# Kernel tuning notes

Hardware: AMD Instinct MI355X
Metric: run time of the kernel (lower is better)

Reference implementation:

```python
import jax, jax.numpy as jnp
import numpy as np

D_MODEL = 1024
NUM_HEADS = 16
D_K = D_MODEL // NUM_HEADS
THETA = 10000.0
BATCH = 2
SEQ = 2048


def setup_inputs() -> dict:
    key = jax.random.key(0)
    ks = jax.random.split(key, 5)
    std = np.sqrt(2.0 / (D_MODEL + D_MODEL))
    return {
        "x": jax.random.normal(ks[0], (BATCH, SEQ, D_MODEL), dtype=jnp.float32),
        "Wq": jax.random.normal(ks[1], (D_MODEL, D_MODEL), dtype=jnp.float32) * std,
        "Wk": jax.random.normal(ks[2], (D_MODEL, D_MODEL), dtype=jnp.float32) * std,
        "Wv": jax.random.normal(ks[3], (D_MODEL, D_MODEL), dtype=jnp.float32) * std,
        "Wo": jax.random.normal(ks[4], (D_MODEL, D_MODEL), dtype=jnp.float32) * std,
        "token_positions": jnp.arange(SEQ, dtype=jnp.int64),
    }


def _apply_rope(t, cos, sin):
    # t: [B, H, S, D_K]; cos/sin: [S, D_K//2]
    # Block-diag 2x2 rotation on consecutive pairs (2k, 2k+1) == elementwise rotation.
    tr = t.reshape(*t.shape[:-1], D_K // 2, 2)
    t0, t1 = tr[..., 0], tr[..., 1]
    o0 = t0 * cos - t1 * sin
    o1 = t0 * sin + t1 * cos
    return jnp.stack([o0, o1], axis=-1).reshape(t.shape)


def reference(x, Wq, Wk, Wv, Wo, token_positions):
    B, S, _ = x.shape
    # projections: custom Linear does x @ W.T
    def split_heads(t):
        return t.reshape(B, S, NUM_HEADS, D_K).transpose(0, 2, 1, 3)  # [B,H,S,Dk]

    q = split_heads(x @ Wq.T)
    k = split_heads(x @ Wk.T)
    v = split_heads(x @ Wv.T)

    # RoPE angle table: theta_ik = pos / THETA**(2k/d_k)
    inv_freq = 1.0 / (THETA ** (2.0 * jnp.arange(D_K // 2, dtype=jnp.float32) / D_K))
    angles = token_positions.astype(jnp.float32)[:, None] * inv_freq[None, :]  # [S, Dk//2]
    cos, sin = jnp.cos(angles), jnp.sin(angles)

    q = _apply_rope(q, cos, sin)
    k = _apply_rope(k, cos, sin)

    scale = 1.0 / np.sqrt(D_K)
    scores = jnp.einsum("bhqd,bhkd->bhqk", q, k) * scale  # [B,H,S,S]
    causal = jnp.tril(jnp.ones((S, S), dtype=bool))
    scores = jnp.where(causal, scores, -jnp.inf)
    attn = jax.nn.softmax(scores, axis=-1)
    out = jnp.einsum("bhqk,bhkd->bhqd", attn, v)  # [B,H,S,Dk]
    out = out.transpose(0, 2, 1, 3).reshape(B, S, D_MODEL)
    return out @ Wo.T
```

## Files before the change

### kernel.cpp

```cpp
#include <hip/hip_runtime.h>
#include <hip/hip_bf16.h>
#include <cstdint>
#include <cstddef>

#define BATCH 2
#define SEQ   2048
#define DM    1024
#define NH    16
#define DK    64
#define LOG2E 1.4426950408889634f

typedef __attribute__((ext_vector_type(8)))  short short8;
typedef __attribute__((ext_vector_type(4)))  float f32x4;
typedef __attribute__((ext_vector_type(16))) float f32x16;
typedef __attribute__((ext_vector_type(4)))  int   i32x4;
typedef __attribute__((ext_vector_type(2)))  int   i32x2;

__device__ __forceinline__ void gload_lds16(const __hip_bfloat16* g, __hip_bfloat16* l) {
  __builtin_amdgcn_global_load_lds((const __attribute__((address_space(1))) void*)g,
                                   (__attribute__((address_space(3))) void*)l, 16, 0, 0);
}

__device__ __forceinline__ int cvtpk_bf16(float lo, float hi) {
  int r;
  asm("v_cvt_pk_bf16_f32 %0, %1, %2" : "=v"(r) : "v"(lo), "v"(hi));
  return r;
}

__device__ __forceinline__ float bf2f(short v) {
  return __int_as_float(((int)(unsigned short)v) << 16);
}

__device__ __forceinline__ float partner32(float x, int hi) {
  auto r = __builtin_amdgcn_permlane32_swap(__float_as_int(x), __float_as_int(x), false, false);
  return __int_as_float(hi ? r[0] : r[1]);
}

__global__ void cast_all(const float* __restrict__ x,  const float* __restrict__ Wq,
                         const float* __restrict__ Wk, const float* __restrict__ Wv,
                         const float* __restrict__ Wo, __hip_bfloat16* __restrict__ dst,
                         const int* __restrict__ pos,  float2* __restrict__ tbl) {
  const int NX = BATCH * SEQ * DM;
  int t = blockIdx.x * 256 + threadIdx.x;
  if (t < SEQ * 32) {
    int s = t >> 5, d2 = t & 31;
    float ang = (float)pos[s] * exp2f(-(float)d2 * 0.415241011860920f);
    float cv, sv;
    __sincosf(ang, &sv, &cv);
    tbl[t] = make_float2(cv, sv);
  }
  size_t i = (size_t)t * 4;
  const float* s;
  if (i < (size_t)NX) {
    s = x + i;
  } else {
    size_t j = i - NX;
    int wsel = (int)(j >> 20);
    size_t o = j & ((1u << 20) - 1);
    s = (wsel == 0 ? Wq : wsel == 1 ? Wk : wsel == 2 ? Wv : Wo) + o;
  }
  float4 v = *(const float4*)s;
  i32x2 pk;
  pk[0] = cvtpk_bf16(v.x, v.y);
  pk[1] = cvtpk_bf16(v.z, v.w);
  *(i32x2*)(dst + i) = pk;
}

template<bool F32OUT, bool VSPLIT>
__global__ __launch_bounds__(256)
void gemm_bt(const __hip_bfloat16* __restrict__ A,
             const __hip_bfloat16* __restrict__ Bw,
             void* __restrict__ Cv, __hip_bfloat16* __restrict__ vt,
             int M, int N, int K, int ldc) {
  __shared__ __hip_bfloat16 As[2][128 * 32];
  __shared__ __hip_bfloat16 Bs[2][128 * 32];
  const int tid  = threadIdx.x;
  const int lane = tid & 63;
  const int w    = tid >> 6;
  const int wr   = w >> 1, wc = w & 1;
  const int g    = lane >> 4;
  const int lr   = lane & 15;

  const int nwg = gridDim.x * gridDim.y;
  const int bid = blockIdx.y * gridDim.x + blockIdx.x;
  const int cpx = nwg >> 3;
  const int sbid = (bid & 7) * cpx + (bid >> 3);
  const int bx = sbid % gridDim.x, by = sbid / gridDim.x;
  const int bm0  = by * 128;
  const int bn0  = bx * 128;

  f32x4 acc[4][4] = {};

  const int strow = lane >> 2;
  const int stcol = (lane & 3) * 8;

  auto STAGE = [&](int buf, int kt) {
    #pragma unroll
    for (int it = 0; it < 2; ++it) {
      int row = (w * 2 + it) * 16 + strow;
      gload_lds16(A  + (size_t)(bm0 + row) * K + kt + stcol, &As[buf][row * 32 + stcol]);
      gload_lds16(Bw + (size_t)(bn0 + row) * K + kt + stcol, &Bs[buf][row * 32 + stcol]);
    }
  };

  STAGE(0, 0);
  __syncthreads();
  int cur = 0;
  const int nk = K / 32;
  for (int ki = 0; ki < nk; ++ki) {
    if (ki + 1 < nk) STAGE(cur ^ 1, (ki + 1) * 32);
    short8 a[4], b[4];
    #pragma unroll
    for (int m = 0; m < 4; ++m)
      a[m] = *(const short8*)(&As[cur][(wr * 64 + m * 16 + lr) * 32 + g * 8]);
    #pragma unroll
    for (int n = 0; n < 4; ++n)
      b[n] = *(const short8*)(&Bs[cur][(wc * 64 + n * 16 + lr) * 32 + g * 8]);
    #pragma unroll
    for (int m = 0; m < 4; ++m)
      #pragma unroll
      for (int n = 0; n < 4; ++n)
        acc[m][n] = __builtin_amdgcn_mfma_f32_16x16x32_bf16(a[m], b[n], acc[m][n], 0, 0, 0);
    __syncthreads();
    cur ^= 1;
  }

  if (VSPLIT && bn0 >= 2048) {
    #pragma unroll
    for (int m = 0; m < 4; ++m)
      #pragma unroll
      for (int n = 0; n < 4; ++n) {
        int nn = bn0 + wc * 64 + n * 16 + lr - 2048;
        int hd = nn >> 6, d = nn & 63;
        int m0 = bm0 + wr * 64 + m * 16 + g * 4;
        int bb = m0 >> 11, ss = m0 & 2047;
        i32x2 pk;
        pk[0] = cvtpk_bf16(acc[m][n][0], acc[m][n][1]);
        pk[1] = cvtpk_bf16(acc[m][n][2], acc[m][n][3]);
        *(i32x2*)(vt + ((size_t)(bb * NH + hd) * DK + d) * SEQ + ss) = pk;
      }
  } else {
    #pragma unroll
    for (int m = 0; m < 4; ++m)
      #pragma unroll
      for (int n = 0; n < 4; ++n) {
        int col = bn0 + wc * 64 + n * 16 + lr;
        #pragma unroll
        for (int r = 0; r < 4; ++r) {
          int row = bm0 + wr * 64 + m * 16 + g * 4 + r;
          float v = acc[m][n][r];
          if (F32OUT) ((float*)Cv)[(size_t)row * ldc + col] = v;
          else        ((__hip_bfloat16*)Cv)[(size_t)row * ldc + col] = __float2bfloat16(v);
        }
      }
  }
}

__global__ void rope_vec(__hip_bfloat16* __restrict__ qk, const float2* __restrict__ tbl) {
  int idx = blockIdx.x * 256 + threadIdx.x;
  int row = idx >> 7;
  int hg  = idx & 127;
  int h   = hg >> 3, gg = hg & 7;
  const float QS = 0.125f * LOG2E;
  size_t base = (size_t)row * 2048 + h * 64 + gg * 8;
  const float2* tp = tbl + (row & (SEQ - 1)) * 32 + gg * 4;
  short8 q = *(const short8*)(qk + base);
  short8 k = *(const short8*)(qk + base + 1024);
  i32x4 qo, ko;
  #pragma unroll
  for (int j = 0; j < 4; ++j) {
    float2 cs = tp[j];
    float q0 = bf2f(q[2 * j]), q1 = bf2f(q[2 * j + 1]);
    float k0 = bf2f(k[2 * j]), k1 = bf2f(k[2 * j + 1]);
    qo[j] = cvtpk_bf16((q0 * cs.x - q1 * cs.y) * QS, (q0 * cs.y + q1 * cs.x) * QS);
    ko[j] = cvtpk_bf16(k0 * cs.x - k1 * cs.y,        k0 * cs.y + k1 * cs.x);
  }
  *(i32x4*)(qk + base)        = qo;
  *(i32x4*)(qk + base + 1024) = ko;
}

__global__ __launch_bounds__(512)
void flash_attn(const __hip_bfloat16* __restrict__ qk,
                const __hip_bfloat16* __restrict__ vt,
                __hip_bfloat16* __restrict__ outb) {
  __shared__ __hip_bfloat16 Kls[2][2][64 * 64];
  __shared__ __hip_bfloat16 Vls[2][2][64 * 64];
  const int pi = blockIdx.x;
  const int NQB = SEQ / 128;
  const int qbh = NQB - 1 - pi, qbl = pi;
  const int hd = blockIdx.y, b = blockIdx.z;
  const int tid = threadIdx.x, lane = tid & 63, w = tid >> 6;
  const int wh = w & 3;
  const int qb_eff = (w < 4) ? qbh : qbl;
  const int hi = lane >> 5, ql = lane & 31;
  const int q0w = qb_eff * 128 + wh * 32;
  const int nph  = qbh + 1;
  const int tmaxw = 2 * qb_eff + (wh >> 1);

  const __hip_bfloat16* Qb = qk + (size_t)(b * SEQ) * 2048 + hd * DK;
  const __hip_bfloat16* Kg = qk + (size_t)(b * SEQ) * 2048 + 1024 + hd * DK;
  const __hip_bfloat16* Vg = vt + (size_t)(b * NH + hd) * DK * SEQ;

  short8 qf[4];
  #pragma unroll
  for (int c = 0; c < 4; ++c)
    qf[c] = *(const short8*)(Qb + (size_t)(q0w + ql) * 2048 + c * 16 + hi * 8);

  f32x16 o0 = {}, o1 = {};
  float m_run = -1e30f, l_run = 0.f;

  const int srow = tid >> 3;
  const int sc0  = (tid & 7) * 8;
  const int swz  = (srow & 7) << 3;

  short8 kr0, kr1, vr0, vr1;
  auto LOAD = [&](int ph) {
    int r0 = ph * 128;
    kr0 = *(const short8*)(Kg + (size_t)(r0 + srow) * 2048 + sc0);
    kr1 = *(const short8*)(Kg + (size_t)(r0 + 64 + srow) * 2048 + sc0);
    vr0 = *(const short8*)(Vg + (size_t)srow * SEQ + r0 + sc0);
    vr1 = *(const short8*)(Vg + (size_t)srow * SEQ + r0 + 64 + sc0);
  };
  auto WRITE = [&](int buf) {
    *(short8*)(&Kls[buf][0][srow * 64 + (sc0 ^ swz)]) = kr0;
    *(short8*)(&Kls[buf][1][srow * 64 + (sc0 ^ swz)]) = kr1;
    *(short8*)(&Vls[buf][0][srow * 64 + (sc0 ^ swz)]) = vr0;
    *(short8*)(&Vls[buf][1][srow * 64 + (sc0 ^ swz)]) = vr1;
  };

  LOAD(0);
  WRITE(0);

  for (int ph = 0; ph < nph; ++ph) {
    const int cur = ph & 1;
    if (ph + 1 < nph) LOAD(ph + 1);
    __syncthreads();

    #pragma unroll
    for (int sub = 0; sub < 2; ++sub) {
      const int tt = 2 * ph + sub;
      if (tt <= tmaxw) {
        f32x16 s0 = {}, s1 = {};
        __builtin_amdgcn_s_setprio(1);
        #pragma unroll
        for (int c = 0; c < 4; ++c) {
          int col = (c * 16 + hi * 8) ^ ((ql & 7) << 3);
          short8 ka = *(const short8*)(&Kls[cur][sub][ql * 64 + col]);
          short8 kb = *(const short8*)(&Kls[cur][sub][(32 + ql) * 64 + col]);
          s0 = __builtin_amdgcn_mfma_f32_32x32x16_bf16(ka, qf[c], s0, 0, 0, 0);
          s1 = __builtin_amdgcn_mfma_f32_32x32x16_bf16(kb, qf[c], s1, 0, 0, 0);
        }
        __builtin_amdgcn_s_setprio(0);

        if (tt * 64 + 63 > q0w) {
          int qg = q0w + ql;
          #pragma unroll
          for (int r = 0; r < 16; ++r) {
            int krow = (r & 3) + 8 * (r >> 2) + 4 * hi;
            if (tt * 64 + krow > qg)      s0[r] = -1e30f;
            if (tt * 64 + 32 + krow > qg) s1[r] = -1e30f;
          }
        }

        float mx = s0[0];
        #pragma unroll
        for (int r = 1; r < 16; ++r) mx = fmaxf(mx, s0[r]);
        #pragma unroll
        for (int r = 0; r < 16; ++r) mx = fmaxf(mx, s1[r]);
        mx = fmaxf(mx, partner32(mx, hi));

        if (!__all(mx <= m_run + 8.f)) {
          float mn  = fmaxf(m_run, mx);
          float fac = __builtin_amdgcn_exp2f(m_run - mn);
          m_run = mn;
          l_run *= fac;
          #pragma unroll
          for (int r = 0; r < 16; ++r) { o0[r] *= fac; o1[r] *= fac; }
        }
        float sum = 0.f;
        #pragma unroll
        for (int r = 0; r < 16; ++r) { s0[r] = __builtin_amdgcn_exp2f(s0[r] - m_run); sum += s0[r]; }
        #pragma unroll
        for (int r = 0; r < 16; ++r) { s1[r] = __builtin_amdgcn_exp2f(s1[r] - m_run); sum += s1[r]; }
        sum += partner32(sum, hi);
        l_run += sum;

        short8 pf[4];
        #pragma unroll
        for (int kt = 0; kt < 2; ++kt) {
          const f32x16& sv = kt ? s1 : s0;
          #pragma unroll
          for (int u = 0; u < 2; ++u) {
            int wa0 = cvtpk_bf16(sv[8 * u + 0], sv[8 * u + 1]);
            int wa1 = cvtpk_bf16(sv[8 * u + 2], sv[8 * u + 3]);
            int wb0 = cvtpk_bf16(sv[8 * u + 4], sv[8 * u + 5]);
            int wb1 = cvtpk_bf16(sv[8 * u + 6], sv[8 * u + 7]);
            auto r0 = __builtin_amdgcn_permlane32_swap(wa0, wb0, false, false);
            auto r1 = __builtin_amdgcn_permlane32_swap(wa1, wb1, false, false);
            i32x4 fr; fr[0] = r0[0]; fr[1] = r1[0]; fr[2] = r0[1]; fr[3] = r1[1];
            pf[kt * 2 + u] = *(short8*)&fr;
          }
        }

        __builtin_amdgcn_s_setprio(1);
        #pragma unroll
        for (int cc = 0; cc < 4; ++cc) {
          int col = (cc * 16 + hi * 8) ^ ((ql & 7) << 3);
          short8 va = *(const short8*)(&Vls[cur][sub][ql * 64 + col]);
          short8 vb = *(const short8*)(&Vls[cur][sub][(32 + ql) * 64 + col]);
          o0 = __builtin_amdgcn_mfma_f32_32x32x16_bf16(va, pf[cc], o0, 0, 0, 0);
          o1 = __builtin_amdgcn_mfma_f32_32x32x16_bf16(vb, pf[cc], o1, 0, 0, 0);
        }
        __builtin_amdgcn_s_setprio(0);
      }
    }

    if (ph + 1 < nph) WRITE(cur ^ 1);
  }

  float inv = 1.f / l_run;
  __hip_bfloat16* orow = outb + (size_t)(b * SEQ + q0w + ql) * DM + hd * DK;
  #pragma unroll
  for (int dt = 0; dt < 2; ++dt) {
    const f32x16& oa = dt ? o1 : o0;
    #pragma unroll
    for (int a = 0; a < 4; ++a) {
      int d0 = dt * 32 + a * 8 + hi * 4;
      i32x2 pk;
      pk[0] = cvtpk_bf16(oa[4 * a + 0] * inv, oa[4 * a + 1] * inv);
      pk[1] = cvtpk_bf16(oa[4 * a + 2] * inv, oa[4 * a + 3] * inv);
      *(i32x2*)(orow + d0) = pk;
    }
  }
}

extern "C" void kernel_launch(void* const* d_in, const int* in_sizes, int n_in,
                              void* d_out, int out_size, void* d_ws, size_t ws_size,
                              hipStream_t stream) {
  const float* x  = (const float*)d_in[0];
  const float* Wq = (const float*)d_in[1];
  const float* Wk = (const float*)d_in[2];
  const float* Wv = (const float*)d_in[3];
  const float* Wo = (const float*)d_in[4];
  const int*   tp = (const int*)d_in[5];
  float* out = (float*)d_out;

  char* ws = (char*)d_ws;
  __hip_bfloat16* xb    = (__hip_bfloat16*)(ws);
  __hip_bfloat16* wqkv  = (__hip_bfloat16*)(ws + (8u  << 20));
  __hip_bfloat16* wob   = (__hip_bfloat16*)(ws + (14u << 20));
  __hip_bfloat16* qkbuf = (__hip_bfloat16*)(ws + (16u << 20));
  __hip_bfloat16* vtbuf = (__hip_bfloat16*)(ws + (32u << 20));
  __hip_bfloat16* attnb = (__hip_bfloat16*)(ws + (40u << 20));
  float2*         tbl   = (float2*)(ws + (40u << 20));

  cast_all<<<8192, 256, 0, stream>>>(x, Wq, Wk, Wv, Wo, xb, tp, tbl);

  gemm_bt<false, true><<<dim3(3 * DM / 128, BATCH * SEQ / 128), 256, 0, stream>>>(
      xb, wqkv, (void*)qkbuf, vtbuf, BATCH * SEQ, 3 * DM, DM, 2048);

  rope_vec<<<(BATCH * SEQ * NH * 8) / 256, 256, 0, stream>>>(qkbuf, tbl);

  flash_attn<<<dim3(SEQ / 256, NH, BATCH), 512, 0, stream>>>(qkbuf, vtbuf, attnb);

  gemm_bt<true, false><<<dim3(DM / 128, BATCH * SEQ / 128), 256, 0, stream>>>(
      attnb, wob, (void*)out, nullptr, BATCH * SEQ, DM, DM, DM);
}
```

Measured before the change: 114.8 us.

## Process both 64-key subtiles per phase with a single online-softmax update

Merges the two 64-key sub-iterations of each phase into one 128-key step. QK^T runs for both subtiles, then one max reduction, one rescale check and one exp/sum pass cover all of them before the PV MFMAs. This halves the number of cross-lane reductions and rescale branches and gives more independent MFMAs to overlap. In exchange it raises register pressure, and waves whose last valid tile is the first subtile now also compute a fully masked second subtile.

```diff
diff --git a/kernel.cpp b/kernel.cpp
--- a/kernel.cpp
+++ b/kernel.cpp
@@ -195,7 +195,6 @@
   const int hi = lane >> 5, ql = lane & 31;
   const int q0w = qb_eff * 128 + wh * 32;
   const int nph  = qbh + 1;
-  const int tmaxw = 2 * qb_eff + (wh >> 1);
 
   const __hip_bfloat16* Qb = qk + (size_t)(b * SEQ) * 2048 + hd * DK;
   const __hip_bfloat16* Kg = qk + (size_t)(b * SEQ) * 2048 + 1024 + hd * DK;
@@ -236,83 +235,121 @@
     if (ph + 1 < nph) LOAD(ph + 1);
     __syncthreads();
 
-    #pragma unroll
-    for (int sub = 0; sub < 2; ++sub) {
-      const int tt = 2 * ph + sub;
-      if (tt <= tmaxw) {
-        f32x16 s0 = {}, s1 = {};
-        __builtin_amdgcn_s_setprio(1);
-        #pragma unroll
-        for (int c = 0; c < 4; ++c) {
-          int col = (c * 16 + hi * 8) ^ ((ql & 7) << 3);
-          short8 ka = *(const short8*)(&Kls[cur][sub][ql * 64 + col]);
-          short8 kb = *(const short8*)(&Kls[cur][sub][(32 + ql) * 64 + col]);
-          s0 = __builtin_amdgcn_mfma_f32_32x32x16_bf16(ka, qf[c], s0, 0, 0, 0);
-          s1 = __builtin_amdgcn_mfma_f32_32x32x16_bf16(kb, qf[c], s1, 0, 0, 0);
+    if (ph <= qb_eff) {
+      const int t0 = 2 * ph, t1 = 2 * ph + 1;
+
+      f32x16 sA0 = {}, sA1 = {}, sB0 = {}, sB1 = {};
+      __builtin_amdgcn_s_setprio(1);
+      #pragma unroll
+      for (int c = 0; c < 4; ++c) {
+        int col = (c * 16 + hi * 8) ^ ((ql & 7) << 3);
+        short8 ka = *(const short8*)(&Kls[cur][0][ql * 64 + col]);
+        short8 kb = *(const short8*)(&Kls[cur][0][(32 + ql) * 64 + col]);
+        short8 kc = *(const short8*)(&Kls[cur][1][ql * 64 + col]);
+        short8 kd = *(const short8*)(&Kls[cur][1][(32 + ql) * 64 + col]);
+        sA0 = __builtin_amdgcn_mfma_f32_32x32x16_bf16(ka, qf[c], sA0, 0, 0, 0);
+        sA1 = __builtin_amdgcn_mfma_f32_32x32x16_bf16(kb, qf[c], sA1, 0, 0, 0);
+        sB0 = __builtin_amdgcn_mfma_f32_32x32x16_bf16(kc, qf[c], sB0, 0, 0, 0);
+        sB1 = __builtin_amdgcn_mfma_f32_32x32x16_bf16(kd, qf[c], sB1, 0, 0, 0);
+      }
+      __builtin_amdgcn_s_setprio(0);
+
+      if (t0 * 64 + 63 > q0w) {
+        int qg = q0w + ql;
+        #pragma unroll
+        for (int r = 0; r < 16; ++r) {
+          int krow = (r & 3) + 8 * (r >> 2) + 4 * hi;
+          if (t0 * 64 + krow > qg)      sA0[r] = -1e30f;
+          if (t0 * 64 + 32 + krow > qg) sA1[r] = -1e30f;
         }
-        __builtin_amdgcn_s_setprio(0);
-
-        if (tt * 64 + 63 > q0w) {
-          int qg = q0w + ql;
-          #pragma unroll
-          for (int r = 0; r < 16; ++r) {
-            int krow = (r & 3) + 8 * (r >> 2) + 4 * hi;
-            if (tt * 64 + krow > qg)      s0[r] = -1e30f;
-            if (tt * 64 + 32 + krow > qg) s1[r] = -1e30f;
-          }
+      }
+      if (t1 * 64 + 63 > q0w) {
+        int qg = q0w + ql;
+        #pragma unroll
+        for (int r = 0; r < 16; ++r) {
+          int krow = (r & 3) + 8 * (r >> 2) + 4 * hi;
+          if (t1 * 64 + krow > qg)      sB0[r] = -1e30f;
+          if (t1 * 64 + 32 + krow > qg) sB1[r] = -1e30f;
         }
-
-        float mx = s0[0];
-        #pragma unroll
-        for (int r = 1; r < 16; ++r) mx = fmaxf(mx, s0[r]);
-        #pragma unroll
-        for (int r = 0; r < 16; ++r) mx = fmaxf(mx, s1[r]);
-        mx = fmaxf(mx, partner32(mx, hi));
-
-        if (!__all(mx <= m_run + 8.f)) {
-          float mn  = fmaxf(m_run, mx);
-          float fac = __builtin_amdgcn_exp2f(m_run - mn);
-          m_run = mn;
-          l_run *= fac;
-          #pragma unroll
-          for (int r = 0; r < 16; ++r) { o0[r] *= fac; o1[r] *= fac; }
+      }
+
+      float mx = sA0[0];
+      #pragma unroll
+      for (int r = 1; r < 16; ++r) mx = fmaxf(mx, sA0[r]);
+      #pragma unroll
+      for (int r = 0; r < 16; ++r) mx = fmaxf(mx, fmaxf(sA1[r], fmaxf(sB0[r], sB1[r])));
+      mx = fmaxf(mx, partner32(mx, hi));
+
+      if (!__all(mx <= m_run + 8.f)) {
+        float mn  = fmaxf(m_run, mx);
+        float fac = __builtin_amdgcn_exp2f(m_run - mn);
+        m_run = mn;
+        l_run *= fac;
+        #pragma unroll
+        for (int r = 0; r < 16; ++r) { o0[r] *= fac; o1[r] *= fac; }
+      }
+      float sum = 0.f;
+      #pragma unroll
+      for (int r = 0; r < 16; ++r) { sA0[r] = __builtin_amdgcn_exp2f(sA0[r] - m_run); sum += sA0[r]; }
+      #pragma unroll
+      for (int r = 0; r < 16; ++r) { sA1[r] = __builtin_amdgcn_exp2f(sA1[r] - m_run); sum += sA1[r]; }
+      #pragma unroll
+      for (int r = 0; r < 16; ++r) { sB0[r] = __builtin_amdgcn_exp2f(sB0[r] - m_run); sum += sB0[r]; }
+      #pragma unroll
+      for (int r = 0; r < 16; ++r) { sB1[r] = __builtin_amdgcn_exp2f(sB1[r] - m_run); sum += sB1[r]; }
+      sum += partner32(sum, hi);
+      l_run += sum;
+
+      short8 pfA[4], pfB[4];
+      #pragma unroll
+      for (int kt = 0; kt < 2; ++kt) {
+        const f32x16& sv = kt ? sA1 : sA0;
+        #pragma unroll
+        for (int u = 0; u < 2; ++u) {
+          int wa0 = cvtpk_bf16(sv[8 * u + 0], sv[8 * u + 1]);
+          int wa1 = cvtpk_bf16(sv[8 * u + 2], sv[8 * u + 3]);
+          int wb0 = cvtpk_bf16(sv[8 * u + 4], sv[8 * u + 5]);
+          int wb1 = cvtpk_bf16(sv[8 * u + 6], sv[8 * u + 7]);
+          auto r0 = __builtin_amdgcn_permlane32_swap(wa0, wb0, false, false);
+          auto r1 = __builtin_amdgcn_permlane32_swap(wa1, wb1, false, false);
+          i32x4 fr; fr[0] = r0[0]; fr[1] = r1[0]; fr[2] = r0[1]; fr[3] = r1[1];
+          pfA[kt * 2 + u] = *(short8*)&fr;
         }
-        float sum = 0.f;
-        #pragma unroll
-        for (int r = 0; r < 16; ++r) { s0[r] = __builtin_amdgcn_exp2f(s0[r] - m_run); sum += s0[r]; }
-        #pragma unroll
-        for (int r = 0; r < 16; ++r) { s1[r] = __builtin_amdgcn_exp2f(s1[r] - m_run); sum += s1[r]; }
-        sum += partner32(sum, hi);
-        l_run += sum;
-
-        short8 pf[4];
-        #pragma unroll
-        for (int kt = 0; kt < 2; ++kt) {
-          const f32x16& sv = kt ? s1 : s0;
-          #pragma unroll
-          for (int u = 0; u < 2; ++u) {
-            int wa0 = cvtpk_bf16(sv[8 * u + 0], sv[8 * u + 1]);
-            int wa1 = cvtpk_bf16(sv[8 * u + 2], sv[8 * u + 3]);
-            int wb0 = cvtpk_bf16(sv[8 * u + 4], sv[8 * u + 5]);
-            int wb1 = cvtpk_bf16(sv[8 * u + 6], sv[8 * u + 7]);
-            auto r0 = __builtin_amdgcn_permlane32_swap(wa0, wb0, false, false);
-            auto r1 = __builtin_amdgcn_permlane32_swap(wa1, wb1, false, false);
-            i32x4 fr; fr[0] = r0[0]; fr[1] = r1[0]; fr[2] = r0[1]; fr[3] = r1[1];
-            pf[kt * 2 + u] = *(short8*)&fr;
-          }
+      }
+      #pragma unroll
+      for (int kt = 0; kt < 2; ++kt) {
+        const f32x16& sv = kt ? sB1 : sB0;
+        #pragma unroll
+        for (int u = 0; u < 2; ++u) {
+          int wa0 = cvtpk_bf16(sv[8 * u + 0], sv[8 * u + 1]);
+          int wa1 = cvtpk_bf16(sv[8 * u + 2], sv[8 * u + 3]);
+          int wb0 = cvtpk_bf16(sv[8 * u + 4], sv[8 * u + 5]);
+          int wb1 = cvtpk_bf16(sv[8 * u + 6], sv[8 * u + 7]);
+          auto r0 = __builtin_amdgcn_permlane32_swap(wa0, wb0, false, false);
+          auto r1 = __builtin_amdgcn_permlane32_swap(wa1, wb1, false, false);
+          i32x4 fr; fr[0] = r0[0]; fr[1] = r1[0]; fr[2] = r0[1]; fr[3] = r1[1];
+          pfB[kt * 2 + u] = *(short8*)&fr;
         }
-
-        __builtin_amdgcn_s_setprio(1);
-        #pragma unroll
-        for (int cc = 0; cc < 4; ++cc) {
-          int col = (cc * 16 + hi * 8) ^ ((ql & 7) << 3);
-          short8 va = *(const short8*)(&Vls[cur][sub][ql * 64 + col]);
-          short8 vb = *(const short8*)(&Vls[cur][sub][(32 + ql) * 64 + col]);
-          o0 = __builtin_amdgcn_mfma_f32_32x32x16_bf16(va, pf[cc], o0, 0, 0, 0);
-          o1 = __builtin_amdgcn_mfma_f32_32x32x16_bf16(vb, pf[cc], o1, 0, 0, 0);
-        }
-        __builtin_amdgcn_s_setprio(0);
-      }
+      }
+
+      __builtin_amdgcn_s_setprio(1);
+      #pragma unroll
+      for (int cc = 0; cc < 4; ++cc) {
+        int col = (cc * 16 + hi * 8) ^ ((ql & 7) << 3);
+        short8 va = *(const short8*)(&Vls[cur][0][ql * 64 + col]);
+        short8 vb = *(const short8*)(&Vls[cur][0][(32 + ql) * 64 + col]);
+        o0 = __builtin_amdgcn_mfma_f32_32x32x16_bf16(va, pfA[cc], o0, 0, 0, 0);
+        o1 = __builtin_amdgcn_mfma_f32_32x32x16_bf16(vb, pfA[cc], o1, 0, 0, 0);
+      }
+      #pragma unroll
+      for (int cc = 0; cc < 4; ++cc) {
+        int col = (cc * 16 + hi * 8) ^ ((ql & 7) << 3);
+        short8 vc = *(const short8*)(&Vls[cur][1][ql * 64 + col]);
+        short8 vd = *(const short8*)(&Vls[cur][1][(32 + ql) * 64 + col]);
+        o0 = __builtin_amdgcn_mfma_f32_32x32x16_bf16(vc, pfB[cc], o0, 0, 0, 0);
+        o1 = __builtin_amdgcn_mfma_f32_32x32x16_bf16(vd, pfB[cc], o1, 0, 0, 0);
+      }
+      __builtin_amdgcn_s_setprio(0);
     }
 
     if (ph + 1 < nph) WRITE(cur ^ 1);
```

After: 114.1 us. About the same (-0.6%).
